# Optimization experiments

Measured on AMD Instinct MI355X. Metric: run time of the kernel, lower is better.

The kernel has to match this reference:

```python
import jax, jax.numpy as jnp
import numpy as np

B, L, H, NH = 4, 2048, 1024, 8
DK = H // NH   # head_k_dim = 128
DV = H // NH   # head_v_dim = 128
CONV_K, FIR_S, FIR_L = 4, 3, 31
CMAX = 0.2
EPS = 1e-5
CHUNK = 32


def _l2norm(x):
    return x * jax.lax.rsqrt(jnp.sum(x * x, -1, keepdims=True) + 1e-6)


def _rms(x, w):
    return x * jax.lax.rsqrt(jnp.mean(x * x, -1, keepdims=True) + EPS) * w


def _causal_conv(x, w):
    # x: [b, l, d], w: [d, K] depthwise causal FIR (ShortConvolution)
    K = w.shape[1]
    l = x.shape[1]
    xp = jnp.pad(x, ((0, 0), (K - 1, 0), (0, 0)))
    return sum(xp[:, i:i + l, :] * w[:, i][None, None, :] for i in range(K))


def _fir(x, w):
    # x: [b, l, h, d], w: [h, d, K] per-head depthwise causal FIR
    K = w.shape[-1]
    l = x.shape[1]
    xp = jnp.pad(x, ((0, 0), (K - 1, 0), (0, 0), (0, 0)))
    return sum(xp[:, i:i + l] * w[:, :, i][None, None] for i in range(K))


def _delta_rule_chunkwise(q, k, v, beta, chunk=CHUNK):
    # q,k: [b,h,L,dk]; v: [b,h,L,dv]; beta: [b,h,L]; L % chunk == 0
    b, h, Ln, dk = q.shape
    dv = v.shape[-1]
    n = Ln // chunk
    q = _l2norm(q)
    k = _l2norm(k)
    v = v * beta[..., None]
    kb = k * beta[..., None]
    rs = lambda t: t.reshape(b, h, n, chunk, t.shape[-1])
    qc, kc, vc, kbc = rs(q), rs(k), rs(v), rs(kb)
    mask_incl = jnp.triu(jnp.ones((chunk, chunk), dtype=bool), 0)
    mask_strict = jnp.triu(jnp.ones((chunk, chunk), dtype=bool), 1)
    # UT / WY transform: sequential Gaussian-elimination over chunk rows
    attn = jnp.where(mask_incl, 0.0, -(kbc @ jnp.swapaxes(kc, -1, -2)))
    for i in range(1, chunk):
        row = attn[..., i, :]                                   # [b,h,n,c]
        upd = jnp.einsum('bhnj,bhnjk->bhnk', row, attn[..., :i])  # [b,h,n,i]
        attn = attn.at[..., i, :i].add(upd)
    attn = attn + jnp.eye(chunk, dtype=attn.dtype)
    u = attn @ vc    # [b,h,n,c,dv]
    w = attn @ kbc   # [b,h,n,c,dk]
    # sequential scan over chunks carrying state S [b,h,dk,dv]
    mv = lambda t: jnp.moveaxis(t, 2, 0)  # [n,b,h,c,d]
    def step(S, xs):
        q_i, k_i, u_i, w_i = xs
        attn_local = jnp.where(mask_strict, 0.0, q_i @ jnp.swapaxes(k_i, -1, -2))
        u_new = u_i - w_i @ S
        o_i = q_i @ S + attn_local @ u_new
        S = S + jnp.swapaxes(k_i, -1, -2) @ u_new
        return S, o_i
    S0 = jnp.zeros((b, h, dk, dv), dtype=q.dtype)
    S, o = jax.lax.scan(step, S0, (mv(qc), mv(kc), mv(u), mv(w)))
    o = jnp.moveaxis(o, 0, 2).reshape(b, h, Ln, dv)
    return o, S


def _forward(hidden_states, Wq, Wk, Wv, Wb, conv_q_w, conv_k_w, conv_v_w,
             fir_short_w, fir_long_w, floor_W, floor_b, fus_W1, fus_b1,
             fus_W2, fus_b2, norm_pf_w, norm_o_w, Wo):
    b, l, _ = hidden_states.shape
    hs = hidden_states
    q_lin = jax.nn.silu(_causal_conv(hs @ Wq, conv_q_w))
    k_lin = jax.nn.silu(_causal_conv(hs @ Wk, conv_k_w))
    v_lin = jax.nn.silu(_causal_conv(hs @ Wv, conv_v_w))
    q = q_lin.reshape(b, l, NH, DK)
    k = k_lin.reshape(b, l, NH, DK)
    v_direct = v_lin.reshape(b, l, NH, DV)
    beta = jax.nn.sigmoid(hs @ Wb)  # [b,l,h]
    delta_out_t, _ = _delta_rule_chunkwise(
        jnp.transpose(q, (0, 2, 1, 3)), jnp.transpose(k, (0, 2, 1, 3)),
        jnp.transpose(v_direct, (0, 2, 1, 3)), jnp.transpose(beta, (0, 2, 1)))
    delta_out = jnp.transpose(delta_out_t, (0, 2, 1, 3))  # [b,l,h,dv]
    local_short = _fir(v_direct, fir_short_w)
    local_long = _fir(v_direct, fir_long_w)
    floor = jax.nn.sigmoid(hs @ floor_W + floor_b) * CMAX  # [b,l,h]
    fus = jax.nn.gelu(hs @ fus_W1 + fus_b1, approximate=False) @ fus_W2 + fus_b2
    fus = fus.reshape(b, l, NH, 4)
    p_value = jax.nn.sigmoid(fus[..., 3]) * (1.0 - floor)  # context share >= floor
    ctx = jax.nn.softmax(fus[..., :3], axis=-1) * (1.0 - p_value)[..., None]
    o = (ctx[..., 0, None] * local_short + ctx[..., 1, None] * local_long
         + ctx[..., 2, None] * delta_out + p_value[..., None] * v_direct)
    o = _rms(o, norm_pf_w)
    o = _rms(o, norm_o_w)
    return o.reshape(b, l, NH * DV) @ Wo


def setup_inputs() -> dict:
    key = jax.random.key(0)
    ks = jax.random.split(key, 16)
    n = lambda k, shape, s=0.02: jax.random.normal(k, shape, jnp.float32) * s
    fus_b2 = jnp.zeros((NH * 4,), jnp.float32).at[3::4].set(4.0)
    return {
        'hidden_states': jax.random.normal(ks[0], (B, L, H), jnp.float32),
        'Wq': n(ks[1], (H, H)), 'Wk': n(ks[2], (H, H)), 'Wv': n(ks[3], (H, H)),
        'Wb': n(ks[4], (H, NH)),
        'conv_q_w': n(ks[5], (H, CONV_K), 0.2),
        'conv_k_w': n(ks[6], (H, CONV_K), 0.2),
        'conv_v_w': n(ks[7], (H, CONV_K), 0.2),
        'fir_short_w': n(ks[8], (NH, DV, FIR_S), 0.2),
        'fir_long_w': n(ks[9], (NH, DV, FIR_L), 0.2),
        'floor_W': n(ks[10], (H, NH)),
        'floor_b': jnp.full((NH,), float(np.log(CMAX / (1 - CMAX))), jnp.float32),
        'fus_W1': n(ks[11], (H, 2 * H)), 'fus_b1': jnp.zeros((2 * H,), jnp.float32),
        'fus_W2': n(ks[12], (2 * H, NH * 4)), 'fus_b2': fus_b2,
        'norm_pf_w': jnp.ones((DV,), jnp.float32),
        'norm_o_w': jnp.ones((DV,), jnp.float32),
        'Wo': n(ks[13], (H, H)),
    }


def reference(hidden_states, Wq, Wk, Wv, Wb, conv_q_w, conv_k_w, conv_v_w,
              fir_short_w, fir_long_w, floor_W, floor_b, fus_W1, fus_b1,
              fus_W2, fus_b2, norm_pf_w, norm_o_w, Wo):
    return _forward(hidden_states, Wq, Wk, Wv, Wb, conv_q_w, conv_k_w, conv_v_w,
                    fir_short_w, fir_long_w, floor_W, floor_b, fus_W1, fus_b1,
                    fus_W2, fus_b2, norm_pf_w, norm_o_w, Wo)
```

## Files before the change

kernel.cpp:

```cpp
#include <hip/hip_runtime.h>
#include <hip/hip_bf16.h>
#include <cstdint>
#include <cstddef>

#define DEVI static __device__ __forceinline__

typedef __attribute__((ext_vector_type(4))) float f32x4;
typedef __attribute__((ext_vector_type(8))) short s16x8;
typedef unsigned short u16;
typedef unsigned int u32;

DEVI float bf2f(u16 u){ u32 x = ((u32)u) << 16; float f; __builtin_memcpy(&f, &x, 4); return f; }
DEVI u16 f2bf(float f){ u32 x; __builtin_memcpy(&x, &f, 4); u32 r = x + 0x7fffu + ((x >> 16) & 1u); return (u16)(r >> 16); }
DEVI float sigm(float x){ return 1.0f / (1.0f + expf(-x)); }
DEVI f32x4 mfma16(s16x8 a, s16x8 b, f32x4 c){ return __builtin_amdgcn_mfma_f32_16x16x32_bf16(a, b, c, 0, 0, 0); }
DEVI s16x8 pack8(float4 a, float4 b){
  s16x8 v;
  v[0]=(short)f2bf(a.x); v[1]=(short)f2bf(a.y); v[2]=(short)f2bf(a.z); v[3]=(short)f2bf(a.w);
  v[4]=(short)f2bf(b.x); v[5]=(short)f2bf(b.y); v[6]=(short)f2bf(b.z); v[7]=(short)f2bf(b.w);
  return v;
}
DEVI s16x8 ld_tr(const u16* p){
  short4 a = *(const short4*)p;
  short4 b = *(const short4*)(p + 4);
  s16x8 v; v[0]=a.x; v[1]=a.y; v[2]=a.z; v[3]=a.w; v[4]=b.x; v[5]=b.y; v[6]=b.z; v[7]=b.w;
  return v;
}

#define GLL16(gp, lp) __builtin_amdgcn_global_load_lds( \
    (const __attribute__((address_space(1))) void*)(gp), \
    (__attribute__((address_space(3))) void*)(lp), 16, 0, 0)

__global__ __launch_bounds__(256) void cvt_bf16_k(const float* __restrict__ src, u16* __restrict__ dst, int n4){
  int i = blockIdx.x * 256 + threadIdx.x;
  if (i < n4){
    float4 v = ((const float4*)src)[i];
    ushort4 o; o.x = f2bf(v.x); o.y = f2bf(v.y); o.z = f2bf(v.z); o.w = f2bf(v.w);
    ((ushort4*)dst)[i] = o;
  }
}

__global__ __launch_bounds__(256) void transpose_bf16_k(const float* __restrict__ src, u16* __restrict__ dst, int K, int N){
  __shared__ float tile[32][33];
  const int n0 = blockIdx.x * 32, k0 = blockIdx.y * 32;
  const int t = threadIdx.x, cc = t & 31, rb = t >> 5;
  #pragma unroll
  for (int it = 0; it < 4; ++it){ int rr = rb + it*8; tile[rr][cc] = src[(size_t)(k0+rr)*N + n0 + cc]; }
  __syncthreads();
  #pragma unroll
  for (int it = 0; it < 4; ++it){ int rr = rb + it*8; dst[(size_t)(n0+rr)*K + k0 + cc] = f2bf(tile[cc][rr]); }
}

__global__ __launch_bounds__(64) void w2pack_k(const float* __restrict__ W2, u16* __restrict__ w2p){
  const int kt = blockIdx.x, nt = blockIdx.y;
  const int lane = threadIdx.x, g = lane >> 4, r = lane & 15;
  float v[8];
  #pragma unroll
  for (int i=0;i<8;++i) v[i] = W2[(size_t)(kt*32 + g*8 + i)*32 + nt*16 + r];
  *(s16x8*)(w2p + (((size_t)kt*2 + nt)*64 + lane)*8) = pack8(make_float4(v[0],v[1],v[2],v[3]),
                                                             make_float4(v[4],v[5],v[6],v[7]));
}

__global__ __launch_bounds__(64) void wbpack_k(const float* __restrict__ Wb, const float* __restrict__ Wfl,
                                              u16* __restrict__ wbp){
  const int kt = blockIdx.x;
  const int lane = threadIdx.x, g = lane >> 4, r = lane & 15;
  float v[8];
  #pragma unroll
  for (int i=0;i<8;++i){
    const int k = kt*32 + g*8 + i;
    v[i] = (r < 8) ? Wb[(size_t)k*8 + r] : Wfl[(size_t)k*8 + (r-8)];
  }
  *(s16x8*)(wbp + ((size_t)kt*64 + lane)*8) = pack8(make_float4(v[0],v[1],v[2],v[3]),
                                                    make_float4(v[4],v[5],v[6],v[7]));
}

template<int EPI>
__global__ __launch_bounds__(256, 2) void gemm_bt(
    const u16* __restrict__ A, const u16* __restrict__ Bt, void* __restrict__ Cout,
    const float* __restrict__ bias, int M, int N, int K)
{
  __shared__ __align__(16) u16 As[128*64];
  __shared__ __align__(16) u16 Bs[128*64];
  const int t = threadIdx.x;
  const int lane = t & 63, w = t >> 6;
  const int wr = w >> 1, wc = w & 1;
  const int g = lane >> 4, r16 = lane & 15;
  const int nwg = gridDim.x * gridDim.y;
  const int bid = blockIdx.x + blockIdx.y * gridDim.x;
  const int swz = (bid & 7) * (nwg >> 3) + (bid >> 3);
  const int m0 = (swz / gridDim.x) * 128, n0 = (swz % gridDim.x) * 128;
  f32x4 acc[4][4];
  #pragma unroll
  for (int i=0;i<4;++i){ f32x4 z = {0,0,0,0}; acc[i][0]=z; acc[i][1]=z; acc[i][2]=z; acc[i][3]=z; }
  const int NK = K / 64;
  const int slot_l = w*64 + lane;
  for (int kt = 0; kt < NK; ++kt){
    __syncthreads();
    #pragma unroll
    for (int j=0;j<4;++j){
      const int sl = j*256 + slot_l;
      const int row = sl >> 3, ch = sl & 7;
      const int chs = ch ^ (row & 7);
      GLL16(A  + (size_t)(m0+row)*K + kt*64 + chs*8, As + (size_t)(j*256 + w*64)*8);
      GLL16(Bt + (size_t)(n0+row)*K + kt*64 + chs*8, Bs + (size_t)(j*256 + w*64)*8);
    }
    __syncthreads();
    #pragma unroll
    for (int kh = 0; kh < 2; ++kh){
      s16x8 af[4], bf_[4];
      #pragma unroll
      for (int i=0;i<4;++i){
        const int arow = wr*64 + i*16 + r16;
        af[i]  = *(const s16x8*)(As + (size_t)arow*64 + (((4*kh+g) ^ (arow&7)))*8);
        const int brow = wc*64 + i*16 + r16;
        bf_[i] = *(const s16x8*)(Bs + (size_t)brow*64 + (((4*kh+g) ^ (brow&7)))*8);
      }
      #pragma unroll
      for (int mi=0;mi<4;++mi)
        #pragma unroll
        for (int ni=0;ni<4;++ni)
          acc[mi][ni] = mfma16(af[mi], bf_[ni], acc[mi][ni]);
    }
  }
  #pragma unroll
  for (int mi=0;mi<4;++mi)
    #pragma unroll
    for (int ni=0;ni<4;++ni){
      const int col = n0 + wc*64 + ni*16 + r16;
      #pragma unroll
      for (int i=0;i<4;++i){
        const int row = m0 + wr*64 + mi*16 + g*4 + i;
        float v = acc[mi][ni][i];
        if (EPI == 0){
          ((u16*)Cout)[(size_t)row*N + col] = f2bf(v);
        } else if (EPI == 1){
          float x = v + bias[col];
          x = 0.5f * x * (1.0f + erff(x * 0.70710678118f));
          ((u16*)Cout)[(size_t)row*N + col] = f2bf(x);
        } else if (EPI == 2){
          ((float*)Cout)[(size_t)row*N + col] = v;
        } else {
          ((u16*)Cout)[(size_t)(col >> 10)*8388608 + (size_t)row*1024 + (col & 1023)] = f2bf(v);
        }
      }
    }
}

__global__ __launch_bounds__(64) void beta_floor_k(
    const u16* __restrict__ hsb, const u16* __restrict__ wbp, const float* __restrict__ flb,
    float* __restrict__ beta, float* __restrict__ flo)
{
  const int m0 = blockIdx.x * 16;
  const int lane = threadIdx.x, g = lane >> 4, r = lane & 15;
  f32x4 acc0 = {0,0,0,0}, acc1 = {0,0,0,0};
  #pragma unroll 4
  for (int kt = 0; kt < 32; kt += 2){
    s16x8 a0 = *(const s16x8*)(hsb + (size_t)(m0+r)*1024 + kt*32 + g*8);
    s16x8 b0 = *(const s16x8*)(wbp + ((size_t)kt*64 + lane)*8);
    s16x8 a1 = *(const s16x8*)(hsb + (size_t)(m0+r)*1024 + (kt+1)*32 + g*8);
    s16x8 b1 = *(const s16x8*)(wbp + ((size_t)(kt+1)*64 + lane)*8);
    acc0 = mfma16(a0, b0, acc0);
    acc1 = mfma16(a1, b1, acc1);
  }
  const float fb = (r >= 8) ? flb[r-8] : 0.f;
  #pragma unroll
  for (int i=0;i<4;++i){
    const int row = m0 + g*4 + i;
    const float v = acc0[i] + acc1[i];
    if (r < 8) beta[(size_t)row*8 + r] = sigm(v);
    else       flo [(size_t)row*8 + (r-8)] = 0.2f * sigm(v + fb);
  }
}

__global__ __launch_bounds__(256) void conv_silu_k(
    const u16* __restrict__ qraw, const u16* __restrict__ kraw, const u16* __restrict__ vraw,
    const float* __restrict__ cwq, const float* __restrict__ cwk, const float* __restrict__ cwv,
    u16* __restrict__ vdir, u16* __restrict__ qn, u16* __restrict__ kn)
{
  const int blk = blockIdx.x;
  const int b = blk >> 7, lt = blk & 127;
  const int l0 = lt * 16;
  const int t = threadIdx.x, c0 = t * 4;
  float wq[16], wk[16], wv[16];
  #pragma unroll
  for (int cc=0; cc<4; ++cc){
    float4 a = *(const float4*)(cwq + (size_t)(c0+cc)*4);
    wq[cc*4+0]=a.x; wq[cc*4+1]=a.y; wq[cc*4+2]=a.z; wq[cc*4+3]=a.w;
    float4 bq = *(const float4*)(cwk + (size_t)(c0+cc)*4);
    wk[cc*4+0]=bq.x; wk[cc*4+1]=bq.y; wk[cc*4+2]=bq.z; wk[cc*4+3]=bq.w;
    float4 c = *(const float4*)(cwv + (size_t)(c0+cc)*4);
    wv[cc*4+0]=c.x; wv[cc*4+1]=c.y; wv[cc*4+2]=c.z; wv[cc*4+3]=c.w;
  }
  float hq[3][4], hk[3][4], hv[3][4];
  #pragma unroll
  for (int i=0;i<3;++i){
    const int ls = l0 - 3 + i;
    if (ls >= 0){
      const size_t base = ((size_t)(b << 11) + ls)*1024 + c0;
      union{ ushort4 v; u16 s[4]; } xq, xk, xv;
      xq.v = *(const ushort4*)(qraw + base);
      xk.v = *(const ushort4*)(kraw + base);
      xv.v = *(const ushort4*)(vraw + base);
      #pragma unroll
      for (int cc=0;cc<4;++cc){ hq[i][cc]=bf2f(xq.s[cc]); hk[i][cc]=bf2f(xk.s[cc]); hv[i][cc]=bf2f(xv.s[cc]); }
    } else {
      #pragma unroll
      for (int cc=0;cc<4;++cc){ hq[i][cc]=0.f; hk[i][cc]=0.f; hv[i][cc]=0.f; }
    }
  }
  float cq[4], ck4[4], cv4[4], nq[4], nk[4], nv[4];
  {
    const size_t base = ((size_t)(b << 11) + l0)*1024 + c0;
    union{ ushort4 v; u16 s[4]; } xq, xk, xv;
    xq.v = *(const ushort4*)(qraw + base);
    xk.v = *(const ushort4*)(kraw + base);
    xv.v = *(const ushort4*)(vraw + base);
    #pragma unroll
    for (int cc=0;cc<4;++cc){ cq[cc]=bf2f(xq.s[cc]); ck4[cc]=bf2f(xk.s[cc]); cv4[cc]=bf2f(xv.s[cc]); }
  }
  const int head = c0 >> 7, d0 = c0 & 127;
  for (int rr = 0; rr < 16; ++rr){
    const int l = l0 + rr;
    if (rr < 15){
      const size_t base = ((size_t)(b << 11) + l + 1)*1024 + c0;
      union{ ushort4 v; u16 s[4]; } xq, xk, xv;
      xq.v = *(const ushort4*)(qraw + base);
      xk.v = *(const ushort4*)(kraw + base);
      xv.v = *(const ushort4*)(vraw + base);
      #pragma unroll
      for (int cc=0;cc<4;++cc){ nq[cc]=bf2f(xq.s[cc]); nk[cc]=bf2f(xk.s[cc]); nv[cc]=bf2f(xv.s[cc]); }
    }
    float qa[4], ka[4], va[4];
    #pragma unroll
    for (int cc=0; cc<4; ++cc){
      qa[cc] = hq[0][cc]*wq[cc*4+0] + hq[1][cc]*wq[cc*4+1] + hq[2][cc]*wq[cc*4+2] + cq[cc]*wq[cc*4+3];
      ka[cc] = hk[0][cc]*wk[cc*4+0] + hk[1][cc]*wk[cc*4+1] + hk[2][cc]*wk[cc*4+2] + ck4[cc]*wk[cc*4+3];
      va[cc] = hv[0][cc]*wv[cc*4+0] + hv[1][cc]*wv[cc*4+1] + hv[2][cc]*wv[cc*4+2] + cv4[cc]*wv[cc*4+3];
    }
    #pragma unroll
    for (int cc=0; cc<4; ++cc){
      qa[cc] = qa[cc]*sigm(qa[cc]); ka[cc] = ka[cc]*sigm(ka[cc]); va[cc] = va[cc]*sigm(va[cc]);
    }
    const int grow = (b << 11) + l;
    ushort4 ov; ov.x=f2bf(va[0]); ov.y=f2bf(va[1]); ov.z=f2bf(va[2]); ov.w=f2bf(va[3]);
    *(ushort4*)(vdir + (size_t)grow*1024 + c0) = ov;
    float ssq = 0.f, ssk = 0.f;
    #pragma unroll
    for (int cc=0; cc<4; ++cc){ ssq += qa[cc]*qa[cc]; ssk += ka[cc]*ka[cc]; }
    #pragma unroll
    for (int m=1; m<32; m<<=1){ ssq += __shfl_xor(ssq, m, 64); ssk += __shfl_xor(ssk, m, 64); }
    const float rq = rsqrtf(ssq + 1e-6f), rk = rsqrtf(ssk + 1e-6f);
    const size_t ob = (((size_t)(b*8 + head))*2048 + l)*128 + d0;
    ushort4 oq, ok;
    oq.x=f2bf(qa[0]*rq); oq.y=f2bf(qa[1]*rq); oq.z=f2bf(qa[2]*rq); oq.w=f2bf(qa[3]*rq);
    ok.x=f2bf(ka[0]*rk); ok.y=f2bf(ka[1]*rk); ok.z=f2bf(ka[2]*rk); ok.w=f2bf(ka[3]*rk);
    *(ushort4*)(qn + ob) = oq;
    *(ushort4*)(kn + ob) = ok;
    #pragma unroll
    for (int cc=0; cc<4; ++cc){
      hq[0][cc]=hq[1][cc]; hq[1][cc]=hq[2][cc]; hq[2][cc]=cq[cc];  cq[cc]=nq[cc];
      hk[0][cc]=hk[1][cc]; hk[1][cc]=hk[2][cc]; hk[2][cc]=ck4[cc]; ck4[cc]=nk[cc];
      hv[0][cc]=hv[1][cc]; hv[1][cc]=hv[2][cc]; hv[2][cc]=cv4[cc]; cv4[cc]=nv[cc];
    }
  }
}

__global__ __launch_bounds__(64) void fus2_k(
    const u16* __restrict__ A, const u16* __restrict__ w2p, const float* __restrict__ b2,
    float* __restrict__ out)
{
  const int m0 = blockIdx.x * 16;
  const int lane = threadIdx.x, g = lane >> 4, r = lane & 15;
  f32x4 acc[2][2];
  #pragma unroll
  for (int nt=0;nt<2;++nt){ f32x4 z = {0,0,0,0}; acc[nt][0]=z; acc[nt][1]=z; }
  #pragma unroll 4
  for (int kt = 0; kt < 64; ++kt){
    s16x8 af = *(const s16x8*)(A + (size_t)(m0+r)*2048 + kt*32 + g*8);
    s16x8 b0 = *(const s16x8*)(w2p + (((size_t)kt*2 + 0)*64 + lane)*8);
    s16x8 b1 = *(const s16x8*)(w2p + (((size_t)kt*2 + 1)*64 + lane)*8);
    acc[0][kt&1] = mfma16(af, b0, acc[0][kt&1]);
    acc[1][kt&1] = mfma16(af, b1, acc[1][kt&1]);
  }
  #pragma unroll
  for (int nt=0;nt<2;++nt){
    const float bb = b2[nt*16 + r];
    #pragma unroll
    for (int i=0;i<4;++i)
      out[(size_t)(m0 + g*4 + i)*32 + nt*16 + r] = acc[nt][0][i] + acc[nt][1][i] + bb;
  }
}

__global__ __launch_bounds__(256, 2) void ut_k(
    const u16* __restrict__ qn, const u16* __restrict__ kn,
    const u16* __restrict__ vdir, const float* __restrict__ beta,
    u16* __restrict__ alocp, u16* __restrict__ updk,
    u16* __restrict__ wpk, u16* __restrict__ knpk)
{
  __shared__ __align__(16) char smem[39680];
  u16*  k_s = (u16*)smem;
  float* Tm = (float*)smem;
  float* Gm = (float*)(smem + 8192);
  float* al = (float*)(smem + 12416);
  float* wl = (float*)(smem + 8192);
  u16*  knT = (u16*)(smem + 17024);
  u16*  vbT = (u16*)(smem + 28288);
  float* bet = (float*)(smem + 39552);

  const int blk = blockIdx.x;
  const int ic = blk & 63, bh = blk >> 6;
  const int b = bh >> 3, h = bh & 7;
  const int l0 = ic * 32;
  const int t = threadIdx.x;
  const int lane = t & 63, w = t >> 6;
  const int g = lane >> 4, r = lane & 15;
  const int mt = w >> 1, nt_g = w & 1;

  const size_t gqk = ((size_t)bh*2048 + l0)*128;

  {
    const int row = t >> 3, sseg = t & 7;
    #pragma unroll
    for (int ss=0; ss<2; ++ss){
      const int s = sseg + ss*8;
      int4 kv = *(const int4*)(kn + gqk + (size_t)row*128 + s*8);
      *(int4*)((char*)k_s + row*256 + ((s ^ (row&7))*16)) = kv;
    }
  }
  {
    const int rp = t & 15, cs = t >> 4;
    const int r0 = 2*rp, r1 = 2*rp + 1;
    union { s16x8 v; u16 u[8]; } k0, k1, v0, v1;
    k0.v = *(const s16x8*)(kn + gqk + (size_t)r0*128 + cs*8);
    k1.v = *(const s16x8*)(kn + gqk + (size_t)r1*128 + cs*8);
    v0.v = *(const s16x8*)(vdir + ((size_t)b*2048 + l0 + r0)*1024 + h*128 + cs*8);
    v1.v = *(const s16x8*)(vdir + ((size_t)b*2048 + l0 + r1)*1024 + h*128 + cs*8);
    const float be0 = beta[((size_t)b*2048 + l0 + r0)*8 + h];
    const float be1 = beta[((size_t)b*2048 + l0 + r1)*8 + h];
    if (t < 32) bet[t] = beta[((size_t)b*2048 + l0 + t)*8 + h];
    #pragma unroll
    for (int i=0;i<8;++i){
      const int d = cs*8 + i;
      *(u32*)(knT + (size_t)d*44 + r0) = (u32)k0.u[i] | ((u32)k1.u[i] << 16);
      u32 lo = f2bf(bf2f(v0.u[i]) * be0);
      u32 hi = f2bf(bf2f(v1.u[i]) * be1);
      *(u32*)(vbT + (size_t)d*44 + r0) = lo | (hi << 16);
    }
  }
  __syncthreads();

  {
    f32x4 gacc = {0,0,0,0}, aacc = {0,0,0,0};
    #pragma unroll
    for (int kt=0; kt<4; ++kt){
      s16x8 afk = *(const s16x8*)(kn + gqk + (size_t)(mt*16+r)*128 + kt*32 + g*8);
      s16x8 afq = *(const s16x8*)(qn + gqk + (size_t)(mt*16+r)*128 + kt*32 + g*8);
      const int brow = nt_g*16 + r;
      s16x8 bfrag = *(const s16x8*)((const char*)k_s + brow*256 + (((kt*4+g) ^ (brow&7))*16));
      gacc = mfma16(afk, bfrag, gacc);
      aacc = mfma16(afq, bfrag, aacc);
    }
    #pragma unroll
    for (int i=0;i<4;++i){
      const int rr = mt*16 + g*4 + i, cc = nt_g*16 + r;
      Gm[rr*33 + cc] = gacc[i];
      al[rr*36 + cc] = (cc <= rr) ? aacc[i] : 0.f;
    }
  }
  __syncthreads();

  if (w == 0){
    const int kk = lane & 15, grp = (lane >> 4) & 1, b0 = grp*16;
    float tc[16];
    #pragma unroll
    for (int j=0;j<16;++j)
      tc[j] = (j > kk) ? (-bet[b0+j] * Gm[(b0+j)*33 + b0+kk]) : 0.f;
    #pragma unroll
    for (int i=1;i<16;++i){
      float upd = 0.f;
      #pragma unroll
      for (int j=0;j<i;++j) upd += __shfl(tc[i], (lane & 48) + j, 64) * tc[j];
      if (kk < i) tc[i] += upd;
    }
    if (lane < 32){
      #pragma unroll
      for (int j=0;j<16;++j) Tm[(b0+j)*36 + b0+kk] = tc[j] + ((j == kk) ? 1.f : 0.f);
      if (grp == 1){
        #pragma unroll
        for (int j=0;j<16;++j) Tm[j*36 + 16 + kk] = 0.f;
      }
    }
  } else if (w == 1){
    #pragma unroll
    for (int m2=0; m2<2; ++m2){
      float4 z0 = *(const float4*)(al + (m2*16+r)*36 + g*8);
      float4 z1 = *(const float4*)(al + (m2*16+r)*36 + g*8 + 4);
      *(s16x8*)(alocp + (((size_t)blk*2 + m2)*64 + lane)*8) = pack8(z0, z1);
    }
  } else {
    #pragma unroll
    for (int q2=0; q2<4; ++q2){
      const int mtd = (w-2)*4 + q2;
      s16x8 vv = ld_tr(knT + (size_t)(mtd*16+r)*44 + g*8);
      *(s16x8*)(knpk + (((size_t)blk*8 + mtd)*64 + lane)*8) = vv;
    }
  }
  __syncthreads();

  {
    const int kP = t >> 4, cP = t & 15;
    float p = 0.f;
    #pragma unroll
    for (int m=0;m<16;++m) p += Gm[(16+kP)*33 + m] * Tm[m*36 + cP];
    al[kP*36 + cP] = -bet[16+kP] * p;
  }
  __syncthreads();

  {
    const int rT = t >> 4, cT = t & 15;
    float s = 0.f;
    #pragma unroll
    for (int k=0;k<16;++k) s += Tm[(16+rT)*36 + 16 + k] * al[k*36 + cT];
    Tm[(16+rT)*36 + cT] = s;
  }
  __syncthreads();

  {
    float bb[8];
    #pragma unroll
    for (int i=0;i<8;++i) bb[i] = bet[g*8+i];
    s16x8 tA[2];
    #pragma unroll
    for (int m2=0; m2<2; ++m2){
      float4 x0 = *(const float4*)(Tm + (m2*16+r)*36 + g*8);
      float4 x1 = *(const float4*)(Tm + (m2*16+r)*36 + g*8 + 4);
      tA[m2] = pack8(x0, x1);
    }
    #pragma unroll
    for (int rr2=0; rr2<2; ++rr2){
      const int nt = rr2*4 + w;
      s16x8 bu   = ld_tr(vbT + (size_t)(nt*16+r)*44 + g*8);
      s16x8 braw = ld_tr(knT + (size_t)(nt*16+r)*44 + g*8);
      s16x8 bw;
      #pragma unroll
      for (int i=0;i<8;++i) bw[i] = (short)f2bf(bf2f((u16)braw[i]) * bb[i]);
      f32x4 zz = {0,0,0,0};
      f32x4 du0 = mfma16(tA[0], bu, zz);
      f32x4 du1 = mfma16(tA[1], bu, zz);
      f32x4 dw0 = mfma16(tA[0], bw, zz);
      f32x4 dw1 = mfma16(tA[1], bw, zz);
      *(s16x8*)(updk + (((size_t)blk*8 + nt)*64 + lane)*8) =
          pack8(make_float4(du0[0],du0[1],du0[2],du0[3]),
                make_float4(du1[0],du1[1],du1[2],du1[3]));
      #pragma unroll
      for (int i=0;i<4;++i){
        wl[(      g*4 + i)*68 + (nt&3)*16 + r] = dw0[i];
        wl[(16 +  g*4 + i)*68 + (nt&3)*16 + r] = dw1[i];
      }
      __syncthreads();
      {
        const int mtp = w >> 1, ktp = rr2*2 + (w & 1);
        float4 y0 = *(const float4*)(wl + (mtp*16+r)*68 + (ktp&1)*32 + g*8);
        float4 y1 = *(const float4*)(wl + (mtp*16+r)*68 + (ktp&1)*32 + g*8 + 4);
        *(s16x8*)(wpk + ((((size_t)blk*2 + mtp)*4 + ktp)*64 + lane)*8) = pack8(y0, y1);
      }
      __syncthreads();
    }
  }
}

struct SBuf {
  s16x8 uraw;
  s16x8 wf[8];
  s16x8 q0[4], q1[4];
  s16x8 a0, a1;
  s16x8 kf[8];
};

DEVI void scan_load(SBuf& b, const u16* up, const u16* wp, const u16* qp,
                    const u16* ap, const u16* kp, int r, int g){
  b.uraw = *(const s16x8*)(up);
  #pragma unroll
  for (int j=0;j<8;++j) b.wf[j] = *(const s16x8*)(wp + j*512);
  #pragma unroll
  for (int kt=0;kt<4;++kt){
    b.q0[kt] = *(const s16x8*)(qp + r*128 + kt*32 + g*8);
    b.q1[kt] = *(const s16x8*)(qp + (16+r)*128 + kt*32 + g*8);
  }
  b.a0 = *(const s16x8*)(ap);
  b.a1 = *(const s16x8*)(ap + 512);
  #pragma unroll
  for (int j=0;j<8;++j) b.kf[j] = *(const s16x8*)(kp + j*512);
}

DEVI void scan_step(const SBuf& b, float* SL, float* UN, f32x4* Sf,
                    u16* dptr, int r, int g){
  s16x8 sf[4];
  #pragma unroll
  for (int kt=0;kt<4;++kt){
    float4 s0 = *(const float4*)&SL[r*132 + kt*32 + g*8];
    float4 s1 = *(const float4*)&SL[r*132 + kt*32 + g*8 + 4];
    sf[kt] = pack8(s0, s1);
  }
  f32x4 acc0, acc1;
  #pragma unroll
  for (int i=0;i<4;++i){
    acc0[i] = -bf2f((u16)b.uraw[i]);
    acc1[i] = -bf2f((u16)b.uraw[4+i]);
  }
  f32x4 o0 = {0,0,0,0}, o1 = {0,0,0,0};
  #pragma unroll
  for (int kt=0;kt<4;++kt){
    acc0 = mfma16(b.wf[kt],   sf[kt], acc0);
    acc1 = mfma16(b.wf[4+kt], sf[kt], acc1);
    o0   = mfma16(b.q0[kt],   sf[kt], o0);
    o1   = mfma16(b.q1[kt],   sf[kt], o1);
  }
  #pragma unroll
  for (int i=0;i<4;++i){
    UN[(g*4+i)*17 + r]    = -acc0[i];
    UN[(16+g*4+i)*17 + r] = -acc1[i];
  }
  s16x8 uf;
  #pragma unroll
  for (int i=0;i<8;++i) uf[i] = (short)f2bf(UN[(g*8+i)*17 + r]);
  o0 = mfma16(b.a0, uf, o0);
  o1 = mfma16(b.a1, uf, o1);
  #pragma unroll
  for (int i=0;i<4;++i){
    dptr[(size_t)(g*4+i)*128]    = f2bf(o0[i]);
    dptr[(size_t)(16+g*4+i)*128] = f2bf(o1[i]);
  }
  #pragma unroll
  for (int m=0;m<8;++m) Sf[m] = mfma16(b.kf[m], uf, Sf[m]);
  #pragma unroll
  for (int m=0;m<8;++m){
    float4 w4 = make_float4(Sf[m][0], Sf[m][1], Sf[m][2], Sf[m][3]);
    *(float4*)&SL[r*132 + m*16 + g*4] = w4;
  }
}

__global__ __launch_bounds__(64, 1) void scan_k(
    const u16* __restrict__ qn, const u16* __restrict__ wpk,
    const u16* __restrict__ updk, const u16* __restrict__ alocp,
    const u16* __restrict__ knpk, u16* __restrict__ delta)
{
  __shared__ float SL[16*132];
  __shared__ float UN[32*17];
  const int blk = blockIdx.x;
  const int sl = blk >> 5, bh = blk & 31;
  const int lane = threadIdx.x;
  const int g = lane >> 4, r = lane & 15;
  for (int i = lane; i < 16*132; i += 64) SL[i] = 0.f;
  f32x4 Sf[8];
  #pragma unroll
  for (int m=0;m<8;++m){ f32x4 z = {0,0,0,0}; Sf[m] = z; }

  const u16* upB = updk + ((size_t)bh*64*8 + sl)*512 + (size_t)lane*8;
  const u16* wpB = wpk  + (size_t)bh*64*4096 + (size_t)lane*8;
  const u16* qpB = qn   + (size_t)bh*2048*128;
  const u16* apB = alocp + (size_t)bh*64*1024 + (size_t)lane*8;
  const u16* kpB = knpk + (size_t)bh*64*4096 + (size_t)lane*8;
  u16*       dB  = delta + (size_t)bh*2048*128 + sl*16 + r;

  SBuf A, B;
  scan_load(A, upB, wpB, qpB, apB, kpB, r, g);
  for (int ic = 0; ic < 64; ic += 2){
    scan_load(B, upB + (size_t)(ic+1)*4096, wpB + (size_t)(ic+1)*4096,
              qpB + (size_t)(ic+1)*4096, apB + (size_t)(ic+1)*1024,
              kpB + (size_t)(ic+1)*4096, r, g);
    scan_step(A, SL, UN, Sf, dB + (size_t)ic*4096, r, g);
    if (ic + 2 < 64)
      scan_load(A, upB + (size_t)(ic+2)*4096, wpB + (size_t)(ic+2)*4096,
                qpB + (size_t)(ic+2)*4096, apB + (size_t)(ic+2)*1024,
                kpB + (size_t)(ic+2)*4096, r, g);
    scan_step(B, SL, UN, Sf, dB + (size_t)(ic+1)*4096, r, g);
  }
}

__global__ __launch_bounds__(256) void fuse_k(
    const u16* __restrict__ vdir, const u16* __restrict__ delta,
    const float* __restrict__ fusv, const float* __restrict__ flo,
    const float* __restrict__ fsw, const float* __restrict__ flw,
    const float* __restrict__ wpf, const float* __restrict__ wno,
    u16* __restrict__ ofin)
{
  __shared__ float vt[94][128];
  __shared__ float fl_s[128*31];
  const int blk = blockIdx.x;
  const int lt = blk & 31, h = (blk >> 5) & 7, b = blk >> 8;
  const int l0 = lt * 64;
  const int t = threadIdx.x;
  for (int i = t; i < 128*31; i += 256) fl_s[i] = flw[(size_t)h*128*31 + i];
  for (int s = t; s < 94*16; s += 256){
    const int rr = s >> 4, cc = (s & 15) * 8;
    const int ls = l0 - 30 + rr;
    if (ls >= 0){
      union { s16x8 v; u16 u[8]; } x;
      x.v = *(const s16x8*)(vdir + ((size_t)b*2048 + ls)*1024 + h*128 + cc);
      *(float4*)&vt[rr][cc]   = make_float4(bf2f(x.u[0]),bf2f(x.u[1]),bf2f(x.u[2]),bf2f(x.u[3]));
      *(float4*)&vt[rr][cc+4] = make_float4(bf2f(x.u[4]),bf2f(x.u[5]),bf2f(x.u[6]),bf2f(x.u[7]));
    } else {
      float4 z = {0,0,0,0};
      *(float4*)&vt[rr][cc] = z; *(float4*)&vt[rr][cc+4] = z;
    }
  }
  __syncthreads();
  const int w = t >> 6, lane = t & 63;
  const int d0 = lane * 2;
  const float wp0 = wpf[d0], wp1 = wpf[d0+1];
  const float wn0 = wno[d0], wn1 = wno[d0+1];
  float fs0[3], fs1[3];
  #pragma unroll
  for (int i=0;i<3;++i){
    fs0[i] = fsw[((size_t)h*128 + d0)*3 + i];
    fs1[i] = fsw[((size_t)h*128 + d0 + 1)*3 + i];
  }
  for (int it = 0; it < 16; ++it){
    const int lr = it*4 + w;
    const int l = l0 + lr;
    const float* fr = fusv + ((size_t)b*2048 + l)*32 + h*4;
    const float f0=fr[0], f1=fr[1], f2=fr[2], f3=fr[3];
    const float flv = flo[((size_t)b*2048 + l)*8 + h];
    const float p = sigm(f3) * (1.f - flv);
    const float mx = fmaxf(f0, fmaxf(f1, f2));
    const float e0 = expf(f0-mx), e1 = expf(f1-mx), e2 = expf(f2-mx);
    const float inv = (1.f - p) / (e0 + e1 + e2);
    const float c0 = e0*inv, c1 = e1*inv, c2 = e2*inv;
    float sh0=0, sh1=0, lg0=0, lg1=0;
    #pragma unroll
    for (int i=0;i<31;++i){
      float2 x = *(const float2*)&vt[lr + i][d0];
      lg0 += x.x * fl_s[d0*31 + i];
      lg1 += x.y * fl_s[(d0+1)*31 + i];
    }
    #pragma unroll
    for (int i=0;i<3;++i){
      float2 x = *(const float2*)&vt[lr + 28 + i][d0];
      sh0 += x.x * fs0[i];
      sh1 += x.y * fs1[i];
    }
    const u32 dl2 = *(const u32*)(delta + (((size_t)(b*8 + h))*2048 + l)*128 + d0);
    const float dlx = bf2f((u16)(dl2 & 0xffffu)), dly = bf2f((u16)(dl2 >> 16));
    float2 vc = *(const float2*)&vt[lr + 30][d0];
    float o0 = c0*sh0 + c1*lg0 + c2*dlx + p*vc.x;
    float o1 = c0*sh1 + c1*lg1 + c2*dly + p*vc.y;
    float ss = o0*o0 + o1*o1;
    #pragma unroll
    for (int m=1; m<64; m<<=1) ss += __shfl_xor(ss, m, 64);
    const float r1 = rsqrtf(ss * (1.f/128.f) + 1e-5f);
    const float a0 = o0*r1*wp0, a1 = o1*r1*wp1;
    float s2 = a0*a0 + a1*a1;
    #pragma unroll
    for (int m=1; m<64; m<<=1) s2 += __shfl_xor(s2, m, 64);
    const float r2 = rsqrtf(s2 * (1.f/128.f) + 1e-5f);
    const u32 h0 = f2bf(a0*r2*wn0), h1 = f2bf(a1*r2*wn1);
    *(u32*)(ofin + ((size_t)b*2048 + l)*1024 + h*128 + d0) = h0 | (h1 << 16);
  }
}

constexpr size_t OFF_HSB  = 0;
constexpr size_t OFF_WQT  = 16777216;
constexpr size_t OFF_WKT  = 18874368;
constexpr size_t OFF_WVT  = 20971520;
constexpr size_t OFF_W1T  = 23068672;
constexpr size_t OFF_WOT  = 27262976;
constexpr size_t OFF_QRAW = 29360128;
constexpr size_t OFF_KRAW = 46137344;
constexpr size_t OFF_VRAW = 62914560;
constexpr size_t OFF_FUSV = 79691776;
constexpr size_t OFF_BETA = 80740352;
constexpr size_t OFF_FLO  = 81002496;
constexpr size_t OFF_VDIR = 81264640;
constexpr size_t OFF_W2P  = 98041856;
constexpr size_t OFF_WBP  = 98172928;
constexpr size_t OFF_QN   = 114819072;
constexpr size_t OFF_KN   = 131596288;
constexpr size_t OFF_ALOC = 148373504;
constexpr size_t OFF_UPDK = 152567808;
constexpr size_t OFF_KNPK = 186122240;

extern "C" void kernel_launch(void* const* d_in, const int* in_sizes, int n_in,
                              void* d_out, int out_size, void* d_ws, size_t ws_size,
                              hipStream_t stream)
{
  const float* hs   = (const float*)d_in[0];
  const float* Wq   = (const float*)d_in[1];
  const float* Wk   = (const float*)d_in[2];
  const float* Wv   = (const float*)d_in[3];
  const float* Wb   = (const float*)d_in[4];
  const float* cq   = (const float*)d_in[5];
  const float* ck   = (const float*)d_in[6];
  const float* cv   = (const float*)d_in[7];
  const float* firs = (const float*)d_in[8];
  const float* firl = (const float*)d_in[9];
  const float* flW  = (const float*)d_in[10];
  const float* flb  = (const float*)d_in[11];
  const float* W1   = (const float*)d_in[12];
  const float* b1   = (const float*)d_in[13];
  const float* W2   = (const float*)d_in[14];
  const float* b2   = (const float*)d_in[15];
  const float* npf  = (const float*)d_in[16];
  const float* now  = (const float*)d_in[17];
  const float* Wo   = (const float*)d_in[18];

  char* ws = (char*)d_ws;
  u16*   hsb   = (u16*)(ws + OFF_HSB);
  u16*   wqT   = (u16*)(ws + OFF_WQT);
  u16*   wkT   = (u16*)(ws + OFF_WKT);
  u16*   wvT   = (u16*)(ws + OFF_WVT);
  u16*   w1T   = (u16*)(ws + OFF_W1T);
  u16*   woT   = (u16*)(ws + OFF_WOT);
  u16*   qraw  = (u16*)(ws + OFF_QRAW);
  u16*   kraw  = (u16*)(ws + OFF_KRAW);
  u16*   vraw  = (u16*)(ws + OFF_VRAW);
  u16*   fus1g = (u16*)(ws + OFF_QRAW);
  float* fusv  = (float*)(ws + OFF_FUSV);
  float* beta  = (float*)(ws + OFF_BETA);
  float* flo   = (float*)(ws + OFF_FLO);
  u16*   vdir  = (u16*)(ws + OFF_VDIR);
  u16*   w2p   = (u16*)(ws + OFF_W2P);
  u16*   wbp   = (u16*)(ws + OFF_WBP);
  u16*   qn    = (u16*)(ws + OFF_QN);
  u16*   kn    = (u16*)(ws + OFF_KN);
  u16*   alocp = (u16*)(ws + OFF_ALOC);
  u16*   updk  = (u16*)(ws + OFF_UPDK);
  u16*   wpk   = (u16*)(ws + OFF_VRAW);
  u16*   knpk  = (u16*)(ws + OFF_KNPK);
  u16*   delta = (u16*)(ws + OFF_QRAW);
  u16*   ofin  = (u16*)(ws + OFF_UPDK);

  cvt_bf16_k<<<8192, 256, 0, stream>>>(hs, hsb, 2097152);
  w2pack_k<<<dim3(64,2), 64, 0, stream>>>(W2, w2p);
  wbpack_k<<<32, 64, 0, stream>>>(Wb, flW, wbp);
  transpose_bf16_k<<<dim3(32,32), 256, 0, stream>>>(Wq, wqT, 1024, 1024);
  transpose_bf16_k<<<dim3(32,32), 256, 0, stream>>>(Wk, wkT, 1024, 1024);
  transpose_bf16_k<<<dim3(32,32), 256, 0, stream>>>(Wv, wvT, 1024, 1024);
  transpose_bf16_k<<<dim3(64,32), 256, 0, stream>>>(W1, w1T, 1024, 2048);
  transpose_bf16_k<<<dim3(32,32), 256, 0, stream>>>(Wo, woT, 1024, 1024);
  beta_floor_k<<<512, 64, 0, stream>>>(hsb, wbp, flb, beta, flo);
  gemm_bt<3><<<dim3(24,64), 256, 0, stream>>>(hsb, wqT, qraw, nullptr, 8192, 3072, 1024);
  conv_silu_k<<<512, 256, 0, stream>>>(qraw, kraw, vraw, cq, ck, cv, vdir, qn, kn);
  gemm_bt<1><<<dim3(16,64), 256, 0, stream>>>(hsb, w1T, fus1g, b1, 8192, 2048, 1024);
  fus2_k<<<512, 64, 0, stream>>>(fus1g, w2p, b2, fusv);
  ut_k<<<2048, 256, 0, stream>>>(qn, kn, vdir, beta, alocp, updk, wpk, knpk);
  scan_k<<<256, 64, 0, stream>>>(qn, wpk, updk, alocp, knpk, delta);
  fuse_k<<<1024, 256, 0, stream>>>(vdir, delta, fusv, flo, firs, firl, npf, now, ofin);
  gemm_bt<2><<<dim3(8,64), 256, 0, stream>>>(ofin, woT, d_out, nullptr, 8192, 1024, 1024);
}
```

Baseline: 371.3 us.

## Keep scan state in registers and redistribute MFMA fragments via wave shuffles

The sequential chunk-scan kernel no longer round-trips the state S and the new-u values through LDS on every step. It packs the fp32 accumulators to bf16 with v_cvt_pk_bf16_f32 and rebuilds the B-operand fragments with cross-lane shuffles. It also folds the sign negation into the precomputed W, so the scan accumulates with positive uraw. It splits the u-new MFMA chain into two independent accumulators to shorten the dependency. The goal is to cut LDS latency on the serial critical path, at the cost of many ds_bpermute shuffles per step.

```diff
diff --git a/kernel.cpp b/kernel.cpp
--- a/kernel.cpp
+++ b/kernel.cpp
@@ -19,6 +19,10 @@
   v[0]=(short)f2bf(a.x); v[1]=(short)f2bf(a.y); v[2]=(short)f2bf(a.z); v[3]=(short)f2bf(a.w);
   v[4]=(short)f2bf(b.x); v[5]=(short)f2bf(b.y); v[6]=(short)f2bf(b.z); v[7]=(short)f2bf(b.w);
   return v;
+}
+DEVI u32 pkbf(float lo, float hi){
+  u32 d; asm("v_cvt_pk_bf16_f32 %0, %1, %2" : "=v"(d) : "v"(lo), "v"(hi));
+  return d;
 }
 DEVI s16x8 ld_tr(const u16* p){
   short4 a = *(const short4*)p;
@@ -455,8 +459,8 @@
                 make_float4(du1[0],du1[1],du1[2],du1[3]));
       #pragma unroll
       for (int i=0;i<4;++i){
-        wl[(      g*4 + i)*68 + (nt&3)*16 + r] = dw0[i];
-        wl[(16 +  g*4 + i)*68 + (nt&3)*16 + r] = dw1[i];
+        wl[(      g*4 + i)*68 + (nt&3)*16 + r] = -dw0[i];
+        wl[(16 +  g*4 + i)*68 + (nt&3)*16 + r] = -dw1[i];
       }
       __syncthreads();
       {
@@ -494,37 +498,59 @@
   for (int j=0;j<8;++j) b.kf[j] = *(const s16x8*)(kp + j*512);
 }
 
-DEVI void scan_step(const SBuf& b, float* SL, float* UN, f32x4* Sf,
-                    u16* dptr, int r, int g){
+DEVI void scan_step(const SBuf& b, f32x4* Sf, u16* dptr,
+                    int srcA, int srcB, bool hi, int r, int g){
+  u32 pk0[8], pk1[8];
+  #pragma unroll
+  for (int m=0;m<8;++m){
+    pk0[m] = pkbf(Sf[m][0], Sf[m][1]);
+    pk1[m] = pkbf(Sf[m][2], Sf[m][3]);
+  }
   s16x8 sf[4];
   #pragma unroll
   for (int kt=0;kt<4;++kt){
-    float4 s0 = *(const float4*)&SL[r*132 + kt*32 + g*8];
-    float4 s1 = *(const float4*)&SL[r*132 + kt*32 + g*8 + 4];
-    sf[kt] = pack8(s0, s1);
-  }
-  f32x4 acc0, acc1;
-  #pragma unroll
-  for (int i=0;i<4;++i){
-    acc0[i] = -bf2f((u16)b.uraw[i]);
-    acc1[i] = -bf2f((u16)b.uraw[4+i]);
-  }
+    u32 eA0 = __shfl(pk0[kt*2],   srcA, 64), oA0 = __shfl(pk0[kt*2+1], srcA, 64);
+    u32 eA1 = __shfl(pk1[kt*2],   srcA, 64), oA1 = __shfl(pk1[kt*2+1], srcA, 64);
+    u32 eB0 = __shfl(pk0[kt*2],   srcB, 64), oB0 = __shfl(pk0[kt*2+1], srcB, 64);
+    u32 eB1 = __shfl(pk1[kt*2],   srcB, 64), oB1 = __shfl(pk1[kt*2+1], srcB, 64);
+    union { u32 w[4]; s16x8 v; } uw;
+    uw.w[0] = hi ? oA0 : eA0;
+    uw.w[1] = hi ? oA1 : eA1;
+    uw.w[2] = hi ? oB0 : eB0;
+    uw.w[3] = hi ? oB1 : eB1;
+    sf[kt] = uw.v;
+  }
+  f32x4 unA, unB, unA2 = {0,0,0,0}, unB2 = {0,0,0,0};
+  #pragma unroll
+  for (int i=0;i<4;++i){ unA[i] = bf2f((u16)b.uraw[i]); unB[i] = bf2f((u16)b.uraw[4+i]); }
+  unA  = mfma16(b.wf[0], sf[0], unA);
+  unA2 = mfma16(b.wf[2], sf[2], unA2);
+  unB  = mfma16(b.wf[4], sf[0], unB);
+  unB2 = mfma16(b.wf[6], sf[2], unB2);
+  unA  = mfma16(b.wf[1], sf[1], unA);
+  unA2 = mfma16(b.wf[3], sf[3], unA2);
+  unB  = mfma16(b.wf[5], sf[1], unB);
+  unB2 = mfma16(b.wf[7], sf[3], unB2);
   f32x4 o0 = {0,0,0,0}, o1 = {0,0,0,0};
   #pragma unroll
   for (int kt=0;kt<4;++kt){
-    acc0 = mfma16(b.wf[kt],   sf[kt], acc0);
-    acc1 = mfma16(b.wf[4+kt], sf[kt], acc1);
-    o0   = mfma16(b.q0[kt],   sf[kt], o0);
-    o1   = mfma16(b.q1[kt],   sf[kt], o1);
-  }
-  #pragma unroll
-  for (int i=0;i<4;++i){
-    UN[(g*4+i)*17 + r]    = -acc0[i];
-    UN[(16+g*4+i)*17 + r] = -acc1[i];
-  }
-  s16x8 uf;
-  #pragma unroll
-  for (int i=0;i<8;++i) uf[i] = (short)f2bf(UN[(g*8+i)*17 + r]);
+    o0 = mfma16(b.q0[kt], sf[kt], o0);
+    o1 = mfma16(b.q1[kt], sf[kt], o1);
+  }
+  unA = unA + unA2;
+  unB = unB + unB2;
+  u32 a0p0 = pkbf(unA[0], unA[1]), a0p1 = pkbf(unA[2], unA[3]);
+  u32 a1p0 = pkbf(unB[0], unB[1]), a1p1 = pkbf(unB[2], unB[3]);
+  u32 w00 = __shfl(a0p0, srcA, 64), w10 = __shfl(a1p0, srcA, 64);
+  u32 w01 = __shfl(a0p1, srcA, 64), w11 = __shfl(a1p1, srcA, 64);
+  u32 w02 = __shfl(a0p0, srcB, 64), w12 = __shfl(a1p0, srcB, 64);
+  u32 w03 = __shfl(a0p1, srcB, 64), w13 = __shfl(a1p1, srcB, 64);
+  union { u32 w[4]; s16x8 v; } uu;
+  uu.w[0] = hi ? w10 : w00;
+  uu.w[1] = hi ? w11 : w01;
+  uu.w[2] = hi ? w12 : w02;
+  uu.w[3] = hi ? w13 : w03;
+  const s16x8 uf = uu.v;
   o0 = mfma16(b.a0, uf, o0);
   o1 = mfma16(b.a1, uf, o1);
   #pragma unroll
@@ -534,11 +560,6 @@
   }
   #pragma unroll
   for (int m=0;m<8;++m) Sf[m] = mfma16(b.kf[m], uf, Sf[m]);
-  #pragma unroll
-  for (int m=0;m<8;++m){
-    float4 w4 = make_float4(Sf[m][0], Sf[m][1], Sf[m][2], Sf[m][3]);
-    *(float4*)&SL[r*132 + m*16 + g*4] = w4;
-  }
 }
 
 __global__ __launch_bounds__(64, 1) void scan_k(
@@ -546,13 +567,13 @@
     const u16* __restrict__ updk, const u16* __restrict__ alocp,
     const u16* __restrict__ knpk, u16* __restrict__ delta)
 {
-  __shared__ float SL[16*132];
-  __shared__ float UN[32*17];
   const int blk = blockIdx.x;
   const int sl = blk >> 5, bh = blk & 31;
   const int lane = threadIdx.x;
   const int g = lane >> 4, r = lane & 15;
-  for (int i = lane; i < 16*132; i += 64) SL[i] = 0.f;
+  const int srcA = (g & 1)*32 + r;
+  const int srcB = srcA + 16;
+  const bool hi = (g >= 2);
   f32x4 Sf[8];
   #pragma unroll
   for (int m=0;m<8;++m){ f32x4 z = {0,0,0,0}; Sf[m] = z; }
@@ -570,12 +591,12 @@
     scan_load(B, upB + (size_t)(ic+1)*4096, wpB + (size_t)(ic+1)*4096,
               qpB + (size_t)(ic+1)*4096, apB + (size_t)(ic+1)*1024,
               kpB + (size_t)(ic+1)*4096, r, g);
-    scan_step(A, SL, UN, Sf, dB + (size_t)ic*4096, r, g);
+    scan_step(A, Sf, dB + (size_t)ic*4096, srcA, srcB, hi, r, g);
     if (ic + 2 < 64)
       scan_load(A, upB + (size_t)(ic+2)*4096, wpB + (size_t)(ic+2)*4096,
                 qpB + (size_t)(ic+2)*4096, apB + (size_t)(ic+2)*1024,
                 kpB + (size_t)(ic+2)*4096, r, g);
-    scan_step(B, SL, UN, Sf, dB + (size_t)(ic+1)*4096, r, g);
+    scan_step(B, Sf, dB + (size_t)(ic+1)*4096, srcA, srcB, hi, r, g);
   }
 }
 
```

Result: no change. 366.1 us (-1.4%).
